# Optimization experiments

Measured on AMD Instinct MI355X. Metric: run time of the kernel, lower is better.

The kernel has to match this reference:

```python
import jax, jax.numpy as jnp
import numpy as np

DEPTH = 2
EPS = 1e-12

def _l2norm(x, axis=-1):
    n = jnp.sqrt(jnp.sum(x * x, axis=axis, keepdims=True))
    return x / jnp.maximum(n, EPS)

def setup_inputs() -> dict:
    key = jax.random.key(0)
    k1, k2, k3, k4, k5 = jax.random.split(key, 5)
    N, D, R, E = 50000, 100, 1000, 800000
    features = jax.random.normal(k1, (N, D), dtype=jnp.float32)
    rel_emb = jax.random.normal(k2, (R, D), dtype=jnp.float32)
    none_relation = jax.random.normal(k3, (D,), dtype=jnp.float32)
    # edge list sorted by destination row (matches coalesced sparse layout
    # assumed by the original: softmax values align with edge order)
    rows = jnp.sort(jax.random.randint(k4, (E,), 0, N))
    cols = jax.random.randint(k5, (E,), 0, N)
    adj_index = jnp.stack([rows, cols], axis=1).astype(jnp.int64)
    return {"features": features, "rel_emb": rel_emb,
            "adj_index": adj_index, "none_relation": none_relation}

def reference(features, rel_emb, adj_index, none_relation):
    N = features.shape[0]
    rows = adj_index[:, 0]  # destination (softmax segment, scatter target)
    cols = adj_index[:, 1]  # neighbor (gather source)
    feats = jnp.tanh(features)
    outputs = [feats]
    nr = _l2norm(none_relation, axis=0)  # [D]
    for _ in range(DEPTH):
        neighs = feats[cols]                      # [E, D] gather
        score = -jnp.einsum('ed,d->e', _l2norm(neighs), nr)  # [E]
        # sparse softmax over each destination row's edges
        m = jax.ops.segment_max(score, rows, num_segments=N)
        e = jnp.exp(score - m[rows])
        denom = jax.ops.segment_sum(e, rows, num_segments=N)
        att = e / denom[rows]                     # [E]
        new_feats = jax.ops.segment_sum(neighs * att[:, None], rows,
                                        num_segments=N)  # [N, D]
        feats = jnp.tanh(new_feats)
        outputs.append(feats)
    return jnp.concatenate(outputs, axis=1)  # [N, D*(DEPTH+1)]
```

## Files before the change

### kernel.cpp

```cpp
#include <hip/hip_runtime.h>
#include <math.h>

#define D_FEAT 100
#define QUARTER 25
#define ROW_STRIDE 300

__device__ __forceinline__ float fast_tanh(float x) {
    float ax = fabsf(x);
    float e  = __expf(2.f * ax);
    float t  = 1.f - 2.f / (e + 1.f);
    return copysignf(t, x);
}

__device__ __forceinline__ unsigned pack_bf16x2(float a, float b) {
    unsigned ua = __float_as_uint(a);
    unsigned ub = __float_as_uint(b);
    ua += 0x7fffu + ((ua >> 16) & 1u);
    ub += 0x7fffu + ((ub >> 16) & 1u);
    return (ua >> 16) | (ub & 0xffff0000u);
}
__device__ __forceinline__ unsigned long long pack_bf16x4(float a, float b,
                                                          float c, float d) {
    return (unsigned long long)pack_bf16x2(a, b) |
           ((unsigned long long)pack_bf16x2(c, d) << 32);
}

template <bool BF16>
__device__ __forceinline__ void gather4(const void* __restrict__ prev, int col,
                                        int l, bool act,
                                        float& x0, float& x1, float& x2, float& x3) {
    x0 = x1 = x2 = x3 = 0.f;
    if (!act) return;
    if (BF16) {
        unsigned long long u =
            ((const unsigned long long*)prev)[(size_t)(unsigned)(col * QUARTER + l)];
        unsigned lo = (unsigned)u, hi = (unsigned)(u >> 32);
        x0 = __uint_as_float(lo << 16);
        x1 = __uint_as_float(lo & 0xffff0000u);
        x2 = __uint_as_float(hi << 16);
        x3 = __uint_as_float(hi & 0xffff0000u);
    } else {
        float4 v = ((const float4*)((const float*)prev + (size_t)col * ROW_STRIDE))[l];
        x0 = v.x; x1 = v.y; x2 = v.z; x3 = v.w;
    }
}

__device__ __forceinline__ float half_reduce(float v) {
    #pragma unroll
    for (int off = 16; off; off >>= 1) v += __shfl_xor(v, off, 64);
    return v;
}

__global__ __launch_bounds__(256) void tanh_score_kernel(
    const float* __restrict__ features,
    float* __restrict__ out,
    unsigned long long* __restrict__ ftab0,
    float* __restrict__ escore0,
    const float* __restrict__ none_rel,
    const int* __restrict__ adj,
    int* __restrict__ startArr,
    int E, int N)
{
    int gtid = blockIdx.x * blockDim.x + threadIdx.x;

    if (gtid <= N) {
        if (gtid == N) startArr[N] = E;
        else {
            int lo = 0, hi = E;
            while (lo < hi) {
                int mid = (lo + hi) >> 1;
                if (adj[2 * mid] < gtid) lo = mid + 1; else hi = mid;
            }
            startArr[gtid] = lo;
        }
    }

    int waveId = gtid >> 6;
    int lane = threadIdx.x & 63;
    int half = lane >> 5;
    int l    = lane & 31;
    int n    = waveId * 2 + half;
    const bool valid_n = (n < N);
    const bool act = valid_n && (l < QUARTER);

    float x0 = 0.f, x1 = 0.f, x2 = 0.f, x3 = 0.f;
    if (act) {
        float4 f = ((const float4*)(features + (size_t)n * D_FEAT))[l];
        x0 = fast_tanh(f.x); x1 = fast_tanh(f.y);
        x2 = fast_tanh(f.z); x3 = fast_tanh(f.w);
        ((float4*)(out + (size_t)n * ROW_STRIDE))[l] = make_float4(x0, x1, x2, x3);
        if (ftab0) ftab0[(size_t)n * QUARTER + l] = pack_bf16x4(x0, x1, x2, x3);
    }

    float nx = 0.f, ny = 0.f, nz = 0.f, nw = 0.f;
    if (l < QUARTER) {
        float4 v = ((const float4*)none_rel)[l];
        nx = v.x; ny = v.y; nz = v.z; nw = v.w;
    }
    float ss = half_reduce(nx * nx + ny * ny + nz * nz + nw * nw);
    float inv_nr = 1.f / fmaxf(sqrtf(ss), 1e-12f);

    float dot = half_reduce(x0 * nx + x1 * ny + x2 * nz + x3 * nw) * inv_nr;
    float sq  = half_reduce(x0 * x0 + x1 * x1 + x2 * x2 + x3 * x3);
    if (l == 0 && valid_n)
        escore0[n] = __expf(-dot / fmaxf(sqrtf(sq), 1e-12f));
}

template <bool BF16>
__global__ __launch_bounds__(256) void attn_kernel(
    const void* __restrict__ prev,
    float* __restrict__ outp,
    unsigned long long* __restrict__ ftab_out,
    const int2* __restrict__ adj2,
    const int* __restrict__ start,
    const float* __restrict__ escore_in,
    float* __restrict__ escore_out,
    const float* __restrict__ none_rel,
    int N)
{
    int waveId = (int)((blockIdx.x * blockDim.x + threadIdx.x) >> 6);
    int lane = threadIdx.x & 63;
    int half = lane >> 5;
    int l    = lane & 31;
    int n    = waveId * 2 + half;
    const bool valid_n = (n < N);
    const bool act = valid_n && (l < QUARTER);
    const int base = half << 5;

    int e0 = 0, e1 = 0;
    if (valid_n) { e0 = start[n]; e1 = start[n + 1]; }
    const int deg = e1 - e0;

    int   c0 = 0, c1 = 0;
    float w0 = 0.f, w1 = 0.f;
    if (l < deg)      { c0 = adj2[e0 + l].y;      w0 = escore_in[c0]; }
    if (l + 32 < deg) { c1 = adj2[e0 + l + 32].y; w1 = escore_in[c1]; }

    int maxdeg = deg;
    { int o = __shfl_xor(maxdeg, 32, 64); maxdeg = maxdeg > o ? maxdeg : o; }

    float a0 = 0.f, a1 = 0.f, a2 = 0.f, a3 = 0.f;
    const int cap1 = maxdeg < 32 ? maxdeg : 32;
    for (int r = 0; r < cap1; r += 8) {
        #pragma unroll
        for (int j = 0; j < 8; ++j) {
            int   i = r + j;
            int   c = __shfl(c0, base + i, 64);
            float w = __shfl(w0, base + i, 64);
            float p0, p1, p2, p3;
            gather4<BF16>(prev, c, l, act && (i < deg), p0, p1, p2, p3);
            a0 += w * p0; a1 += w * p1; a2 += w * p2; a3 += w * p3;
        }
    }
    const int cap2 = maxdeg < 64 ? maxdeg : 64;
    for (int r = 32; r < cap2; r += 8) {
        #pragma unroll
        for (int j = 0; j < 8; ++j) {
            int   i = r + j;
            int   c = __shfl(c1, base + i - 32, 64);
            float w = __shfl(w1, base + i - 32, 64);
            float p0, p1, p2, p3;
            gather4<BF16>(prev, c, l, act && (i < deg), p0, p1, p2, p3);
            a0 += w * p0; a1 += w * p1; a2 += w * p2; a3 += w * p3;
        }
    }
    for (int e = e0 + 64; e < e1; ++e) {
        int   c = adj2[e].y;
        float w = escore_in[c];
        float p0, p1, p2, p3;
        gather4<BF16>(prev, c, l, act, p0, p1, p2, p3);
        a0 += w * p0; a1 += w * p1; a2 += w * p2; a3 += w * p3;
    }

    float d_l = w0 + w1;
    for (int e = e0 + 64 + l; e < e1; e += 32) d_l += escore_in[adj2[e].y];
    d_l = half_reduce(d_l);
    const float inv_d = (deg > 0) ? 1.f / d_l : 0.f;

    float r0 = fast_tanh(a0 * inv_d);
    float r1 = fast_tanh(a1 * inv_d);
    float r2 = fast_tanh(a2 * inv_d);
    float r3 = fast_tanh(a3 * inv_d);
    if (act) {
        ((float4*)(outp + (size_t)n * ROW_STRIDE))[l] = make_float4(r0, r1, r2, r3);
        if (ftab_out) ftab_out[(size_t)n * QUARTER + l] = pack_bf16x4(r0, r1, r2, r3);
    } else {
        r0 = r1 = r2 = r3 = 0.f;
    }

    if (escore_out) {
        float nx = 0.f, ny = 0.f, nz = 0.f, nw = 0.f;
        if (l < QUARTER) {
            float4 v = ((const float4*)none_rel)[l];
            nx = v.x; ny = v.y; nz = v.z; nw = v.w;
        }
        float ss = half_reduce(nx * nx + ny * ny + nz * nz + nw * nw);
        float inv_nr = 1.f / fmaxf(sqrtf(ss), 1e-12f);
        float dot = half_reduce(r0 * nx + r1 * ny + r2 * nz + r3 * nw) * inv_nr;
        float sq  = half_reduce(r0 * r0 + r1 * r1 + r2 * r2 + r3 * r3);
        if (l == 0 && valid_n)
            escore_out[n] = __expf(-dot / fmaxf(sqrtf(sq), 1e-12f));
    }
}

extern "C" void kernel_launch(void* const* d_in, const int* in_sizes, int n_in,
                              void* d_out, int out_size, void* d_ws, size_t ws_size,
                              hipStream_t stream) {
    const float* features = (const float*)d_in[0];
    const int*   adj      = (const int*)d_in[2];
    const float* none_rel = (const float*)d_in[3];
    float* out = (float*)d_out;

    const int N = in_sizes[0] / D_FEAT;
    const int E = in_sizes[2] / 2;

    size_t off = 0;
    auto take = [&](size_t bytes) { size_t o = off; off = (off + bytes + 15) & ~(size_t)15; return o; };
    char* w = (char*)d_ws;
    int*   start   = (int*)  (w + take(sizeof(int)   * (size_t)(N + 1)));
    float* escore0 = (float*)(w + take(sizeof(float) * (size_t)N));
    float* escore1 = (float*)(w + take(sizeof(float) * (size_t)N));
    size_t ftab_off0 = take(sizeof(unsigned long long) * (size_t)N * QUARTER);
    size_t ftab_off1 = take(sizeof(unsigned long long) * (size_t)N * QUARTER);
    const bool use_bf16 = (ws_size >= off);
    unsigned long long* ftab0 = use_bf16 ? (unsigned long long*)(w + ftab_off0) : nullptr;
    unsigned long long* ftab1 = use_bf16 ? (unsigned long long*)(w + ftab_off1) : nullptr;

    const int pairs = (N + 1) / 2;
    const int node_blocks = (pairs * 64 + 255) / 256;
    const int2* adj2 = (const int2*)adj;

    tanh_score_kernel<<<node_blocks, 256, 0, stream>>>(features, out, ftab0,
                                                       escore0, none_rel,
                                                       adj, start, E, N);
    if (use_bf16) {
        attn_kernel<true><<<node_blocks, 256, 0, stream>>>(
            ftab0, out + D_FEAT, ftab1, adj2, start, escore0, escore1, none_rel, N);
        attn_kernel<true><<<node_blocks, 256, 0, stream>>>(
            ftab1, out + 2 * D_FEAT, nullptr, adj2, start, escore1, nullptr, none_rel, N);
    } else {
        attn_kernel<false><<<node_blocks, 256, 0, stream>>>(
            out, out + D_FEAT, nullptr, adj2, start, escore0, escore1, none_rel, N);
        attn_kernel<false><<<node_blocks, 256, 0, stream>>>(
            out + D_FEAT, out + 2 * D_FEAT, nullptr, adj2, start, escore1, nullptr, none_rel, N);
    }
}
```

Before: 184.1 us.

## Embed per-node exp-score in slot zero of the bf16 gather table row

Each bf16 feature-table row grows to 26 u64 slots. Slot 0 holds the node's exp-score, so one row gather gives both the weight (shuffled from lane 0) and the features. This removes the separate escore_in gather per edge and the second pass over edges for the denominator, which is now accumulated inside the main loop. In exchange every row is 8 bytes wider and the denominator is summed serially per edge rather than in parallel across lanes.

```diff
diff --git a/kernel.cpp b/kernel.cpp
--- a/kernel.cpp
+++ b/kernel.cpp
@@ -2,8 +2,8 @@
 #include <math.h>
 
 #define D_FEAT 100
-#define QUARTER 25
 #define ROW_STRIDE 300
+#define ROWQ 26
 
 __device__ __forceinline__ float fast_tanh(float x) {
     float ax = fabsf(x);
@@ -24,25 +24,14 @@
     return (unsigned long long)pack_bf16x2(a, b) |
            ((unsigned long long)pack_bf16x2(c, d) << 32);
 }
-
-template <bool BF16>
-__device__ __forceinline__ void gather4(const void* __restrict__ prev, int col,
-                                        int l, bool act,
-                                        float& x0, float& x1, float& x2, float& x3) {
-    x0 = x1 = x2 = x3 = 0.f;
-    if (!act) return;
-    if (BF16) {
-        unsigned long long u =
-            ((const unsigned long long*)prev)[(size_t)(unsigned)(col * QUARTER + l)];
-        unsigned lo = (unsigned)u, hi = (unsigned)(u >> 32);
-        x0 = __uint_as_float(lo << 16);
-        x1 = __uint_as_float(lo & 0xffff0000u);
-        x2 = __uint_as_float(hi << 16);
-        x3 = __uint_as_float(hi & 0xffff0000u);
-    } else {
-        float4 v = ((const float4*)((const float*)prev + (size_t)col * ROW_STRIDE))[l];
-        x0 = v.x; x1 = v.y; x2 = v.z; x3 = v.w;
-    }
+__device__ __forceinline__ void unpack_bf16x4(unsigned long long u,
+                                              float& x0, float& x1,
+                                              float& x2, float& x3) {
+    unsigned lo = (unsigned)u, hi = (unsigned)(u >> 32);
+    x0 = __uint_as_float(lo << 16);
+    x1 = __uint_as_float(lo & 0xffff0000u);
+    x2 = __uint_as_float(hi << 16);
+    x3 = __uint_as_float(hi & 0xffff0000u);
 }
 
 __device__ __forceinline__ float half_reduce(float v) {
@@ -54,7 +43,7 @@
 __global__ __launch_bounds__(256) void tanh_score_kernel(
     const float* __restrict__ features,
     float* __restrict__ out,
-    unsigned long long* __restrict__ ftab0,
+    unsigned long long* __restrict__ tab0,
     float* __restrict__ escore0,
     const float* __restrict__ none_rel,
     const int* __restrict__ adj,
@@ -62,7 +51,6 @@
     int E, int N)
 {
     int gtid = blockIdx.x * blockDim.x + threadIdx.x;
-
     if (gtid <= N) {
         if (gtid == N) startArr[N] = E;
         else {
@@ -81,20 +69,20 @@
     int l    = lane & 31;
     int n    = waveId * 2 + half;
     const bool valid_n = (n < N);
-    const bool act = valid_n && (l < QUARTER);
+    const bool fact = valid_n && (l >= 1) && (l <= 25);
 
     float x0 = 0.f, x1 = 0.f, x2 = 0.f, x3 = 0.f;
-    if (act) {
-        float4 f = ((const float4*)(features + (size_t)n * D_FEAT))[l];
+    if (fact) {
+        float4 f = ((const float4*)(features + (size_t)n * D_FEAT))[l - 1];
         x0 = fast_tanh(f.x); x1 = fast_tanh(f.y);
         x2 = fast_tanh(f.z); x3 = fast_tanh(f.w);
-        ((float4*)(out + (size_t)n * ROW_STRIDE))[l] = make_float4(x0, x1, x2, x3);
-        if (ftab0) ftab0[(size_t)n * QUARTER + l] = pack_bf16x4(x0, x1, x2, x3);
+        ((float4*)(out + (size_t)n * ROW_STRIDE))[l - 1] = make_float4(x0, x1, x2, x3);
+        if (tab0) tab0[(size_t)n * ROWQ + l] = pack_bf16x4(x0, x1, x2, x3);
     }
 
     float nx = 0.f, ny = 0.f, nz = 0.f, nw = 0.f;
-    if (l < QUARTER) {
-        float4 v = ((const float4*)none_rel)[l];
+    if (l >= 1 && l <= 25) {
+        float4 v = ((const float4*)none_rel)[l - 1];
         nx = v.x; ny = v.y; nz = v.z; nw = v.w;
     }
     float ss = half_reduce(nx * nx + ny * ny + nz * nz + nw * nw);
@@ -102,15 +90,18 @@
 
     float dot = half_reduce(x0 * nx + x1 * ny + x2 * nz + x3 * nw) * inv_nr;
     float sq  = half_reduce(x0 * x0 + x1 * x1 + x2 * x2 + x3 * x3);
-    if (l == 0 && valid_n)
-        escore0[n] = __expf(-dot / fmaxf(sqrtf(sq), 1e-12f));
-}
-
-template <bool BF16>
+    if (l == 0 && valid_n) {
+        float es = __expf(-dot / fmaxf(sqrtf(sq), 1e-12f));
+        if (tab0) tab0[(size_t)n * ROWQ] = (unsigned long long)__float_as_uint(es);
+        else      escore0[n] = es;
+    }
+}
+
+template <bool TAB>
 __global__ __launch_bounds__(256) void attn_kernel(
     const void* __restrict__ prev,
     float* __restrict__ outp,
-    unsigned long long* __restrict__ ftab_out,
+    unsigned long long* __restrict__ tab_out,
     const int2* __restrict__ adj2,
     const int* __restrict__ start,
     const float* __restrict__ escore_in,
@@ -124,7 +115,7 @@
     int l    = lane & 31;
     int n    = waveId * 2 + half;
     const bool valid_n = (n < N);
-    const bool act = valid_n && (l < QUARTER);
+    const bool fact = valid_n && (l >= 1) && (l <= 25);
     const int base = half << 5;
 
     int e0 = 0, e1 = 0;
@@ -133,22 +124,38 @@
 
     int   c0 = 0, c1 = 0;
     float w0 = 0.f, w1 = 0.f;
-    if (l < deg)      { c0 = adj2[e0 + l].y;      w0 = escore_in[c0]; }
-    if (l + 32 < deg) { c1 = adj2[e0 + l + 32].y; w1 = escore_in[c1]; }
+    if (l < deg)      { c0 = adj2[e0 + l].y;      if (!TAB) w0 = escore_in[c0]; }
+    if (l + 32 < deg) { c1 = adj2[e0 + l + 32].y; if (!TAB) w1 = escore_in[c1]; }
 
     int maxdeg = deg;
     { int o = __shfl_xor(maxdeg, 32, 64); maxdeg = maxdeg > o ? maxdeg : o; }
 
-    float a0 = 0.f, a1 = 0.f, a2 = 0.f, a3 = 0.f;
+    const unsigned long long* tab = (const unsigned long long*)prev;
+    const float* pf32 = (const float*)prev;
+
+    float d_acc = 0.f, a0 = 0.f, a1 = 0.f, a2 = 0.f, a3 = 0.f;
     const int cap1 = maxdeg < 32 ? maxdeg : 32;
     for (int r = 0; r < cap1; r += 8) {
         #pragma unroll
         for (int j = 0; j < 8; ++j) {
             int   i = r + j;
             int   c = __shfl(c0, base + i, 64);
-            float w = __shfl(w0, base + i, 64);
-            float p0, p1, p2, p3;
-            gather4<BF16>(prev, c, l, act && (i < deg), p0, p1, p2, p3);
+            float w, p0, p1, p2, p3;
+            if (TAB) {
+                bool on = valid_n && (i < deg) && (l <= 25);
+                unsigned long long v = 0;
+                if (on) v = tab[(size_t)(unsigned)(c * ROWQ + l)];
+                w = __shfl(__uint_as_float((unsigned)v), base, 64);
+                unpack_bf16x4(v, p0, p1, p2, p3);
+            } else {
+                w = __shfl(w0, base + i, 64);
+                p0 = p1 = p2 = p3 = 0.f;
+                if (fact && (i < deg)) {
+                    float4 v = ((const float4*)(pf32 + (size_t)c * ROW_STRIDE))[l - 1];
+                    p0 = v.x; p1 = v.y; p2 = v.z; p3 = v.w;
+                }
+            }
+            d_acc += w;
             a0 += w * p0; a1 += w * p1; a2 += w * p2; a3 += w * p3;
         }
     }
@@ -158,48 +165,73 @@
         for (int j = 0; j < 8; ++j) {
             int   i = r + j;
             int   c = __shfl(c1, base + i - 32, 64);
-            float w = __shfl(w1, base + i - 32, 64);
-            float p0, p1, p2, p3;
-            gather4<BF16>(prev, c, l, act && (i < deg), p0, p1, p2, p3);
+            float w, p0, p1, p2, p3;
+            if (TAB) {
+                bool on = valid_n && (i < deg) && (l <= 25);
+                unsigned long long v = 0;
+                if (on) v = tab[(size_t)(unsigned)(c * ROWQ + l)];
+                w = __shfl(__uint_as_float((unsigned)v), base, 64);
+                unpack_bf16x4(v, p0, p1, p2, p3);
+            } else {
+                w = __shfl(w1, base + i - 32, 64);
+                p0 = p1 = p2 = p3 = 0.f;
+                if (fact && (i < deg)) {
+                    float4 v = ((const float4*)(pf32 + (size_t)c * ROW_STRIDE))[l - 1];
+                    p0 = v.x; p1 = v.y; p2 = v.z; p3 = v.w;
+                }
+            }
+            d_acc += w;
             a0 += w * p0; a1 += w * p1; a2 += w * p2; a3 += w * p3;
         }
     }
     for (int e = e0 + 64; e < e1; ++e) {
-        int   c = adj2[e].y;
-        float w = escore_in[c];
-        float p0, p1, p2, p3;
-        gather4<BF16>(prev, c, l, act, p0, p1, p2, p3);
+        int c = adj2[e].y;
+        float w, p0, p1, p2, p3;
+        if (TAB) {
+            unsigned long long v = 0;
+            if (l <= 25) v = tab[(size_t)(unsigned)(c * ROWQ + l)];
+            w = __shfl(__uint_as_float((unsigned)v), base, 64);
+            unpack_bf16x4(v, p0, p1, p2, p3);
+        } else {
+            w = escore_in[c];
+            p0 = p1 = p2 = p3 = 0.f;
+            if (fact) {
+                float4 v = ((const float4*)(pf32 + (size_t)c * ROW_STRIDE))[l - 1];
+                p0 = v.x; p1 = v.y; p2 = v.z; p3 = v.w;
+            }
+        }
+        d_acc += w;
         a0 += w * p0; a1 += w * p1; a2 += w * p2; a3 += w * p3;
     }
 
-    float d_l = w0 + w1;
-    for (int e = e0 + 64 + l; e < e1; e += 32) d_l += escore_in[adj2[e].y];
-    d_l = half_reduce(d_l);
-    const float inv_d = (deg > 0) ? 1.f / d_l : 0.f;
-
+    const float inv_d = (deg > 0) ? 1.f / d_acc : 0.f;
     float r0 = fast_tanh(a0 * inv_d);
     float r1 = fast_tanh(a1 * inv_d);
     float r2 = fast_tanh(a2 * inv_d);
     float r3 = fast_tanh(a3 * inv_d);
-    if (act) {
-        ((float4*)(outp + (size_t)n * ROW_STRIDE))[l] = make_float4(r0, r1, r2, r3);
-        if (ftab_out) ftab_out[(size_t)n * QUARTER + l] = pack_bf16x4(r0, r1, r2, r3);
+    if (fact) {
+        ((float4*)(outp + (size_t)n * ROW_STRIDE))[l - 1] = make_float4(r0, r1, r2, r3);
+        if (TAB && tab_out)
+            tab_out[(size_t)n * ROWQ + l] = pack_bf16x4(r0, r1, r2, r3);
     } else {
         r0 = r1 = r2 = r3 = 0.f;
     }
 
-    if (escore_out) {
+    if (tab_out || escore_out) {
         float nx = 0.f, ny = 0.f, nz = 0.f, nw = 0.f;
-        if (l < QUARTER) {
-            float4 v = ((const float4*)none_rel)[l];
+        if (l >= 1 && l <= 25) {
+            float4 v = ((const float4*)none_rel)[l - 1];
             nx = v.x; ny = v.y; nz = v.z; nw = v.w;
         }
         float ss = half_reduce(nx * nx + ny * ny + nz * nz + nw * nw);
         float inv_nr = 1.f / fmaxf(sqrtf(ss), 1e-12f);
         float dot = half_reduce(r0 * nx + r1 * ny + r2 * nz + r3 * nw) * inv_nr;
         float sq  = half_reduce(r0 * r0 + r1 * r1 + r2 * r2 + r3 * r3);
-        if (l == 0 && valid_n)
-            escore_out[n] = __expf(-dot / fmaxf(sqrtf(sq), 1e-12f));
+        if (l == 0 && valid_n) {
+            float es = __expf(-dot / fmaxf(sqrtf(sq), 1e-12f));
+            if (TAB) tab_out[(size_t)n * ROWQ] = (unsigned long long)__float_as_uint(es);
+            else     escore_out[n] = es;
+        }
     }
 }
 
@@ -220,24 +252,24 @@
     int*   start   = (int*)  (w + take(sizeof(int)   * (size_t)(N + 1)));
     float* escore0 = (float*)(w + take(sizeof(float) * (size_t)N));
     float* escore1 = (float*)(w + take(sizeof(float) * (size_t)N));
-    size_t ftab_off0 = take(sizeof(unsigned long long) * (size_t)N * QUARTER);
-    size_t ftab_off1 = take(sizeof(unsigned long long) * (size_t)N * QUARTER);
-    const bool use_bf16 = (ws_size >= off);
-    unsigned long long* ftab0 = use_bf16 ? (unsigned long long*)(w + ftab_off0) : nullptr;
-    unsigned long long* ftab1 = use_bf16 ? (unsigned long long*)(w + ftab_off1) : nullptr;
+    size_t tab_off0 = take(sizeof(unsigned long long) * (size_t)N * ROWQ);
+    size_t tab_off1 = take(sizeof(unsigned long long) * (size_t)N * ROWQ);
+    const bool use_tab = (ws_size >= off);
+    unsigned long long* tab0 = use_tab ? (unsigned long long*)(w + tab_off0) : nullptr;
+    unsigned long long* tab1 = use_tab ? (unsigned long long*)(w + tab_off1) : nullptr;
 
     const int pairs = (N + 1) / 2;
     const int node_blocks = (pairs * 64 + 255) / 256;
     const int2* adj2 = (const int2*)adj;
 
-    tanh_score_kernel<<<node_blocks, 256, 0, stream>>>(features, out, ftab0,
+    tanh_score_kernel<<<node_blocks, 256, 0, stream>>>(features, out, tab0,
                                                        escore0, none_rel,
                                                        adj, start, E, N);
-    if (use_bf16) {
+    if (use_tab) {
         attn_kernel<true><<<node_blocks, 256, 0, stream>>>(
-            ftab0, out + D_FEAT, ftab1, adj2, start, escore0, escore1, none_rel, N);
+            tab0, out + D_FEAT, tab1, adj2, start, nullptr, nullptr, none_rel, N);
         attn_kernel<true><<<node_blocks, 256, 0, stream>>>(
-            ftab1, out + 2 * D_FEAT, nullptr, adj2, start, escore1, nullptr, none_rel, N);
+            tab1, out + 2 * D_FEAT, nullptr, adj2, start, nullptr, nullptr, none_rel, N);
     } else {
         attn_kernel<false><<<node_blocks, 256, 0, stream>>>(
             out, out + D_FEAT, nullptr, adj2, start, escore0, escore1, none_rel, N);
```

After: 175.5 us. -4.7%, faster.
